# Kernel tuning notes

Measured on AMD Instinct MI355X. Metric: run time of the kernel, lower is better.

The kernel has to match this reference:

```python
import jax, jax.numpy as jnp
import numpy as np

EPS = 1e-06


def setup_inputs() -> dict:
    key = jax.random.key(0)
    k1, k2, k3 = jax.random.split(key, 3)
    N, L, H, D = 2, 2048, 8, 64
    return {
        "queries": jax.random.normal(k1, (N, L, H, D), dtype=jnp.float32),
        "keys": jax.random.normal(k2, (N, L, H, D), dtype=jnp.float32),
        "values": jax.random.normal(k3, (N, L, H, D), dtype=jnp.float32),
    }


def reference(queries, keys, values):
    # [N, L, H, D] -> [N, H, L, D]
    q = jnp.transpose(queries, (0, 2, 1, 3))
    k = jnp.transpose(keys, (0, 2, 1, 3))
    v = jnp.transpose(values, (0, 2, 1, 3))
    # kernel_method = sigmoid (applied to q and k only)
    q = jax.nn.sigmoid(q)
    k = jax.nn.sigmoid(k)
    L = q.shape[2]
    normal = (jnp.arange(L, dtype=q.dtype) + 1.0)[None, None, :]  # [1,1,L]

    sink_incoming = 1.0 / jnp.einsum('nhld,nhld->nhl', q + EPS, jnp.cumsum(k, axis=2) + EPS)
    source_outgoing = 1.0 / jnp.einsum('nhld,nhld->nhl', k + EPS, jnp.cumsum(q, axis=2) + EPS)
    sink_incoming = sink_incoming * normal
    source_outgoing = source_outgoing * normal

    conserved_sink = jnp.einsum(
        'nhld,nhld->nhl', q + EPS,
        jnp.cumsum(k * source_outgoing[..., None], axis=2) + EPS) / normal
    conserved_source = jnp.einsum(
        'nhld,nhld->nhl', k + EPS,
        jnp.cumsum(q * sink_incoming[..., None], axis=2) + EPS) / normal
    conserved_source = jnp.clip(conserved_source, -1.0, 1.0)

    sink_allocation = jax.nn.sigmoid(conserved_sink)
    conserved_source = jnp.exp(conserved_source)
    source_competition = conserved_source / jnp.cumsum(conserved_source, axis=-1) * normal

    # causal dot product: outer-product cumsum as in the original
    q_scaled = q * (sink_incoming / normal)[..., None]
    v_scaled = v * source_competition[..., None]
    kv = jnp.cumsum(jnp.einsum('nhld,nhlm->nhldm', k, v_scaled), axis=2)  # [N,H,L,D,M]
    qkv = jnp.einsum('nhld,nhldm->nhlm', q_scaled, kv)
    x = qkv * sink_allocation[..., None]
    # back to [N, L, H, M]
    return jnp.transpose(x, (0, 2, 1, 3))
```

## Files before the change

kernel.cpp:

```cpp
#include <hip/hip_runtime.h>
#include <math.h>

constexpr int Nn = 2, Hh = 8, Ll = 2048, Dd = 64;
constexpr int S  = Nn * Hh;
constexpr int C  = 64;
constexpr int NC = Ll / C;
constexpr int SC = S * NC;

constexpr int SB  = 72;
constexpr int SRP = 65;
constexpr int SS8 = 9;

#define EPSF 1e-6f
#define FLAG_MAGIC 0x5F3A9D21u

typedef __attribute__((ext_vector_type(8))) short short8;
typedef __attribute__((ext_vector_type(4))) float f32x4;
#define MFMA16(a, b, c) __builtin_amdgcn_mfma_f32_16x16x32_bf16(a, b, c, 0, 0, 0)

__device__ __forceinline__ float rcpf(float x) { return __builtin_amdgcn_rcpf(x); }
__device__ __forceinline__ float sigf(float x) { return rcpf(1.0f + __expf(-x)); }

__device__ __forceinline__ float waveRed(float v) {
#pragma unroll
    for (int off = 32; off > 0; off >>= 1) v += __shfl_xor(v, off, 64);
    return v;
}

__device__ __forceinline__ int gidx(int n, int l, int h, int d) {
    return ((n * Ll + l) * Hh + h) * Dd + d;
}

__device__ __forceinline__ float fc(const float4& v, int u) { return ((const float*)&v)[u]; }

__device__ __forceinline__ unsigned short f2bf(float x) {
    unsigned int u = __float_as_uint(x);
    unsigned int r = (u + 0x7fffu + ((u >> 16) & 1u)) >> 16;
    return (unsigned short)r;
}
__device__ __forceinline__ unsigned int pack2(float lo, float hi) {
    return (unsigned int)f2bf(lo) | ((unsigned int)f2bf(hi) << 16);
}
__device__ __forceinline__ float bf2f(unsigned short u) {
    return __uint_as_float(((unsigned int)u) << 16);
}
__device__ __forceinline__ float lo16(unsigned int x) { return __uint_as_float(x << 16); }
__device__ __forceinline__ float hi16(unsigned int x) { return __uint_as_float(x & 0xffff0000u); }
__device__ __forceinline__ void unpack8(const uint4& v, float* o) {
    o[0] = lo16(v.x); o[1] = hi16(v.x); o[2] = lo16(v.y); o[3] = hi16(v.y);
    o[4] = lo16(v.z); o[5] = hi16(v.z); o[6] = lo16(v.w); o[7] = hi16(v.w);
}

__device__ __forceinline__ void pubf(float* p, float v) {
    __hip_atomic_store((unsigned int*)p, __float_as_uint(v),
                       __ATOMIC_RELAXED, __HIP_MEMORY_SCOPE_AGENT);
}
__device__ __forceinline__ float rdf(const float* p) {
    return __uint_as_float(__hip_atomic_load((const unsigned int*)p,
                       __ATOMIC_RELAXED, __HIP_MEMORY_SCOPE_AGENT));
}
__device__ __forceinline__ void pubu(unsigned int* p, unsigned int v) {
    __hip_atomic_store(p, v, __ATOMIC_RELAXED, __HIP_MEMORY_SCOPE_AGENT);
}
__device__ __forceinline__ unsigned long long rd64(const void* p) {
    return __hip_atomic_load((const unsigned long long*)p,
                             __ATOMIC_RELAXED, __HIP_MEMORY_SCOPE_AGENT);
}
__device__ __forceinline__ void publish_flag(unsigned int* f, int t) {
    asm volatile("s_waitcnt vmcnt(0)" ::: "memory");
    __syncthreads();
    if (t == 0)
        __hip_atomic_store(f, FLAG_MAGIC, __ATOMIC_RELAXED, __HIP_MEMORY_SCOPE_AGENT);
}
__device__ __forceinline__ void wait_n(const unsigned int* f, int n, int t) {
    if (t < 64) {
        const bool need = (t < n);
        for (;;) {
            unsigned int v = need
                ? __hip_atomic_load(&f[t], __ATOMIC_RELAXED, __HIP_MEMORY_SCOPE_AGENT)
                : FLAG_MAGIC;
            if (__all(v == FLAG_MAGIC)) break;
            __builtin_amdgcn_s_sleep(8);
        }
    }
    __syncthreads();
}

__global__ __launch_bounds__(256, 2) void k_all(
        const float* __restrict__ Q, const float* __restrict__ K,
        const float* __restrict__ V,
        float* __restrict__ SK, float* __restrict__ SQ,
        float* __restrict__ SKso, float* __restrict__ SQsi,
        float* __restrict__ Tcs, float* __restrict__ KVT,
        unsigned short* __restrict__ KVpb, float* __restrict__ Out,
        unsigned int* __restrict__ f0, unsigned int* __restrict__ f1,
        unsigned int* __restrict__ f2, unsigned int* __restrict__ f3,
        unsigned int* __restrict__ f4) {
    __shared__ __align__(16) unsigned short sqB[C * SB];
    __shared__ __align__(16) unsigned short skB[C * SB];
    __shared__ __align__(16) unsigned short vsT[C * SB];
    __shared__ __align__(16) unsigned short stB[C * SB];
    __shared__ __align__(16) float Pun[4608];
    __shared__ float scrA[C * SS8], scrB[C * SS8];
    __shared__ float colK[C], colQ[C], pk[Dd], pq[Dd];
    __shared__ float lsi[C], lso[C], rw1[C], rw2[C], le[C], ecum[C], lsc[C], s2l[C];
    __shared__ float pcsv;

    const int b = blockIdx.x, s = b / NC, c = b % NC;
    const int n = s / Hh, h = s % Hh, t = threadIdx.x;
    const int w = t >> 6, lane = t & 63, mf = lane & 15, qq = lane >> 4;
    const int I0 = 16 * w;
    float* P = Pun;

    {
        int d0 = (4 * t) & 63, ig = t >> 4;
        float psk[4] = {0, 0, 0, 0}, psq[4] = {0, 0, 0, 0};
#pragma unroll
        for (int j = 0; j < 4; j++) {
            int i = ig + 16 * j;
            int id = gidx(n, c * C + i, h, d0);
            float4 q4 = *(const float4*)&Q[id];
            float4 k4 = *(const float4*)&K[id];
            float a0 = sigf(q4.x), a1 = sigf(q4.y), a2 = sigf(q4.z), a3 = sigf(q4.w);
            float b0 = sigf(k4.x), b1 = sigf(k4.y), b2 = sigf(k4.z), b3 = sigf(k4.w);
            *(uint2*)&sqB[i * SB + d0] = make_uint2(pack2(a0, a1), pack2(a2, a3));
            *(uint2*)&skB[i * SB + d0] = make_uint2(pack2(b0, b1), pack2(b2, b3));
            psq[0] += a0; psq[1] += a1; psq[2] += a2; psq[3] += a3;
            psk[0] += b0; psk[1] += b1; psk[2] += b2; psk[3] += b3;
        }
#pragma unroll
        for (int r = 0; r < 4; r++) {
            P[ig * 64 + d0 + r] = psk[r];
            P[1024 + ig * 64 + d0 + r] = psq[r];
        }
        int i0 = (t & 15) * 4, dt = (t >> 4) * 4;
        float4 vr[4];
#pragma unroll
        for (int r = 0; r < 4; r++)
            vr[r] = *(const float4*)&V[gidx(n, c * C + i0 + r, h, dt)];
#pragma unroll
        for (int u = 0; u < 4; u++)
            *(uint2*)&vsT[(dt + u) * SB + i0] = make_uint2(
                pack2(fc(vr[0], u), fc(vr[1], u)), pack2(fc(vr[2], u), fc(vr[3], u)));
    }
    __syncthreads();
    if (t < 64) {
        float v = 0.f;
#pragma unroll
        for (int g = 0; g < 16; g++) v += P[g * 64 + t];
        pubf(&SK[b * 64 + t], v);
    } else if (t < 128) {
        int d = t - 64; float v = 0.f;
#pragma unroll
        for (int g = 0; g < 16; g++) v += P[1024 + g * 64 + d];
        pubf(&SQ[b * 64 + d], v);
    }
    publish_flag(&f0[b], t);

    wait_n(&f0[s * NC], c, t);

    {
        int d = t & 63, g = t >> 6;
        float pa = 0.f, pb = 0.f;
#pragma unroll
        for (int u = 0; u < 8; u++) {
            int cp = g + 4 * u;
            float va = rdf(&SK[(s * NC + cp) * 64 + d]);
            float vb = rdf(&SQ[(s * NC + cp) * 64 + d]);
            pa += (cp < c) ? va : 0.f;
            pb += (cp < c) ? vb : 0.f;
        }
        P[2048 + g * 64 + d] = pa;
        P[2304 + g * 64 + d] = pb;
    }
#pragma unroll
    for (int j = 0; j < 2; j++) {
        int flat = 8 * t + 2048 * j, i = flat >> 6, d0 = flat & 63;
        uint4 xq = *(const uint4*)&sqB[i * SB + d0];
        uint4 xk = *(const uint4*)&skB[i * SB + d0];
        float qa[8], ka[8];
        unpack8(xq, qa); unpack8(xk, ka);
        float sq = 0.f, sk = 0.f;
#pragma unroll
        for (int u = 0; u < 8; u++) { sq += qa[u]; sk += ka[u]; }
        scrB[i * SS8 + (d0 >> 3)] = sq;
        scrA[i * SS8 + (d0 >> 3)] = sk;
    }
    __syncthreads();
    if (t < 64) {
        float v = 0.f;
#pragma unroll
        for (int u = 0; u < 8; u++) v += scrA[t * SS8 + u];
        colK[t] = v;
    } else if (t < 128) {
        int i = t - 64; float v = 0.f;
#pragma unroll
        for (int u = 0; u < 8; u++) v += scrB[i * SS8 + u];
        colQ[i] = v;
    } else if (t < 192) {
        int d = t - 128;
        pk[d] = P[2048 + d] + P[2112 + d] + P[2176 + d] + P[2240 + d];
    } else {
        int d = t - 192;
        pq[d] = P[2304 + d] + P[2368 + d] + P[2432 + d] + P[2496 + d];
    }
    __syncthreads();

    {
        f32x4 acc[4] = {{0,0,0,0},{0,0,0,0},{0,0,0,0},{0,0,0,0}};
#pragma unroll
        for (int kk = 0; kk < 64; kk += 32) {
            short8 a = *(const short8*)&sqB[(I0 + mf) * SB + kk + qq * 8];
#pragma unroll
            for (int J = 0; J < 4; J++) {
                short8 bb = *(const short8*)&skB[(16 * J + mf) * SB + kk + qq * 8];
                acc[J] = MFMA16(a, bb, acc[J]);
            }
        }
#pragma unroll
        for (int J = 0; J < 4; J++)
#pragma unroll
            for (int r = 0; r < 4; r++)
                P[(I0 + 4 * qq + r) * SRP + 16 * J + mf] = acc[J][r];
    }
    __syncthreads();

    {
        int i = t >> 2, g = t & 3, l = c * C + i;
        float r1 = 0.f, r2 = 0.f;
#pragma unroll
        for (int u = 0; u < 16; u++) {
            int jj = g + 4 * u;
            float t1 = P[i * SRP + jj] + EPSF * colK[jj];
            float t2 = P[jj * SRP + i] + EPSF * colQ[jj];
            bool ok = (jj <= i);
            r1 += ok ? t1 : 0.f;
            r2 += ok ? t2 : 0.f;
        }
        float b1 = 0.f, b2 = 0.f;
#pragma unroll
        for (int u = 0; u < 16; u++) {
            int d = g * 16 + u;
            b1 += (bf2f(sqB[i * SB + d]) + EPSF) * (pk[d] + EPSF);
            b2 += (bf2f(skB[i * SB + d]) + EPSF) * (pq[d] + EPSF);
        }
        r1 += __shfl_xor(r1, 1, 64); r1 += __shfl_xor(r1, 2, 64);
        r2 += __shfl_xor(r2, 1, 64); r2 += __shfl_xor(r2, 2, 64);
        b1 += __shfl_xor(b1, 1, 64); b1 += __shfl_xor(b1, 2, 64);
        b2 += __shfl_xor(b2, 1, 64); b2 += __shfl_xor(b2, 2, 64);
        if (g == 0) {
            float nf = (float)(l + 1);
            lsi[i] = nf * rcpf(b1 + r1);
            lso[i] = nf * rcpf(b2 + r2);
        }
    }
    __syncthreads();

    {
        int i = t >> 2, g = t & 3;
        float a1 = 0.f, a2 = 0.f;
#pragma unroll
        for (int u = 0; u < 16; u++) {
            int jj = g + 4 * u;
            float t1 = lso[jj] * (P[i * SRP + jj] + EPSF * colK[jj]);
            float t2 = lsi[jj] * (P[jj * SRP + i] + EPSF * colQ[jj]);
            bool ok = (jj <= i);
            a1 += ok ? t1 : 0.f;
            a2 += ok ? t2 : 0.f;
        }
        a1 += __shfl_xor(a1, 1, 64); a1 += __shfl_xor(a1, 2, 64);
        a2 += __shfl_xor(a2, 1, 64); a2 += __shfl_xor(a2, 2, 64);
        if (g == 0) { rw1[i] = a1; rw2[i] = a2; }
    }
    {
        int d = t >> 2, g = t & 3;
        float v1 = 0.f, v2 = 0.f;
#pragma unroll
        for (int u = 0; u < 16; u++) {
            int i = g * 16 + u;
            v1 += bf2f(skB[i * SB + d]) * lso[i];
            v2 += bf2f(sqB[i * SB + d]) * lsi[i];
        }
        v1 += __shfl_xor(v1, 1, 64); v1 += __shfl_xor(v1, 2, 64);
        v2 += __shfl_xor(v2, 1, 64); v2 += __shfl_xor(v2, 2, 64);
        if (g == 0) {
            pubf(&SKso[b * 64 + d], v1);
            pubf(&SQsi[b * 64 + d], v2);
        }
    }
    publish_flag(&f1[b], t);

    wait_n(&f1[s * NC], c, t);

    {
        int d = t & 63, g = t >> 6;
        float pa = 0.f, pb = 0.f;
#pragma unroll
        for (int u = 0; u < 8; u++) {
            int cp = g + 4 * u;
            float va = rdf(&SKso[(s * NC + cp) * 64 + d]);
            float vb = rdf(&SQsi[(s * NC + cp) * 64 + d]);
            pa += (cp < c) ? va : 0.f;
            pb += (cp < c) ? vb : 0.f;
        }
        scrA[g * 64 + d] = pa;
        scrA[256 + g * 64 + d] = pb;
    }
    __syncthreads();
    if (t < 64) pk[t] = scrA[t] + scrA[64 + t] + scrA[128 + t] + scrA[192 + t];
    else if (t < 128) {
        int d = t - 64;
        pq[d] = scrA[256 + d] + scrA[320 + d] + scrA[384 + d] + scrA[448 + d];
    }
    __syncthreads();
    {
        int i = t >> 2, g = t & 3, l = c * C + i;
        float b1 = 0.f, b2 = 0.f;
#pragma unroll
        for (int j = 0; j < 2; j++) {
            uint4 xq = *(const uint4*)&sqB[i * SB + g * 16 + 8 * j];
            uint4 xk = *(const uint4*)&skB[i * SB + g * 16 + 8 * j];
            float qa[8], ka[8];
            unpack8(xq, qa); unpack8(xk, ka);
            int d = g * 16 + 8 * j;
#pragma unroll
            for (int u = 0; u < 8; u++) {
                b1 += (qa[u] + EPSF) * (pk[d + u] + EPSF);
                b2 += (ka[u] + EPSF) * (pq[d + u] + EPSF);
            }
        }
        b1 += __shfl_xor(b1, 1, 64); b1 += __shfl_xor(b1, 2, 64);
        b2 += __shfl_xor(b2, 1, 64); b2 += __shfl_xor(b2, 2, 64);
        if (g == 0) {
            float nf = (float)(l + 1);
            float cs  = (b1 + rw1[i]) * rcpf(nf);
            float csr = (b2 + rw2[i]) * rcpf(nf);
            csr = fminf(fmaxf(csr, -1.f), 1.f);
            float e = __expf(csr);
            float sal = sigf(cs);
            s2l[i] = lsi[i] * rcpf(nf) * sal;
            le[i] = e;
        }
    }
    __syncthreads();
    if (t < 64) {
        float run = le[t];
#pragma unroll
        for (int off = 1; off < 64; off <<= 1) {
            float o = __shfl_up(run, off, 64);
            if (t >= off) run += o;
        }
        ecum[t] = run;
        if (t == 63) pubf(&Tcs[b], run);
    }
    publish_flag(&f2[b], t);

    wait_n(&f2[s * NC], c, t);

    if (t < 64) {
        float v = (t < c) ? rdf(&Tcs[s * NC + t]) : 0.f;
        v = waveRed(v);
        if (t == 0) pcsv = v;
    }
    __syncthreads();
    if (t < 64) {
        int l = c * C + t;
        lsc[t] = le[t] * rcpf(pcsv + ecum[t]) * (float)(l + 1);
    }
    __syncthreads();

    {
        int i = t >> 2, g = t & 3;
        unsigned int wds[8];
#pragma unroll
        for (int p = 0; p < 8; p++) {
            int j0 = g * 16 + 2 * p;
            float v0 = (j0     <= i) ? P[i * SRP + j0]     * lsc[j0]     : 0.f;
            float v1 = (j0 + 1 <= i) ? P[i * SRP + j0 + 1] * lsc[j0 + 1] : 0.f;
            wds[p] = pack2(v0, v1);
        }
        *(uint4*)&stB[i * SB + g * 16]     = make_uint4(wds[0], wds[1], wds[2], wds[3]);
        *(uint4*)&stB[i * SB + g * 16 + 8] = make_uint4(wds[4], wds[5], wds[6], wds[7]);
    }
    __syncthreads();

    unsigned short* skT = (unsigned short*)Pun;
    unsigned short* vsV = (unsigned short*)(Pun + 2304);
#pragma unroll
    for (int j = 0; j < 2; j++) {
        int flat = 8 * t + 2048 * j, dR = flat >> 6, i0 = flat & 63;
        uint4 vv = *(const uint4*)&vsT[dR * SB + i0];
        float x[8];
        unpack8(vv, x);
#pragma unroll
        for (int u = 0; u < 8; u++) x[u] *= lsc[i0 + u];
        uint4 o;
        o.x = pack2(x[0], x[1]); o.y = pack2(x[2], x[3]);
        o.z = pack2(x[4], x[5]); o.w = pack2(x[6], x[7]);
        *(uint4*)&vsV[dR * SB + i0] = o;
    }
    {
        int i0 = (t & 15) * 4, dt = (t >> 4) * 4;
        uint2 kr[4];
#pragma unroll
        for (int r = 0; r < 4; r++) kr[r] = *(const uint2*)&skB[(i0 + r) * SB + dt];
#pragma unroll
        for (int u = 0; u < 4; u++) {
            unsigned int e0 = (u < 2 ? kr[0].x : kr[0].y), e1 = (u < 2 ? kr[1].x : kr[1].y);
            unsigned int e2 = (u < 2 ? kr[2].x : kr[2].y), e3 = (u < 2 ? kr[3].x : kr[3].y);
            int sh = (u & 1) * 16;
            unsigned int lo = ((e0 >> sh) & 0xffffu) | (((e1 >> sh) & 0xffffu) << 16);
            unsigned int hi = ((e2 >> sh) & 0xffffu) | (((e3 >> sh) & 0xffffu) << 16);
            *(uint2*)&skT[(dt + u) * SB + i0] = make_uint2(lo, hi);
        }
    }
    __syncthreads();

    {
        f32x4 acc[4] = {{0,0,0,0},{0,0,0,0},{0,0,0,0},{0,0,0,0}};
#pragma unroll
        for (int kk = 0; kk < 64; kk += 32) {
            short8 a = *(const short8*)&vsV[(I0 + mf) * SB + kk + qq * 8];
#pragma unroll
            for (int J = 0; J < 4; J++) {
                short8 bb = *(const short8*)&skT[(16 * J + mf) * SB + kk + qq * 8];
                acc[J] = MFMA16(a, bb, acc[J]);
            }
        }
#pragma unroll
        for (int J = 0; J < 4; J++)
#pragma unroll
            for (int r = 0; r < 4; r++)
                pubf(&KVT[(size_t)b * 4096 + (I0 + 4 * qq + r) * 64 + 16 * J + mf],
                     acc[J][r]);
    }
    publish_flag(&f3[b], t);

    if (b < 128) {
        int sp = b >> 3, sub = b & 7;
        wait_n(&f3[sp * NC], NC, t);
        int e0 = sub * 512 + 2 * t;
        float2 x[NC];
#pragma unroll
        for (int cp = 0; cp < NC; cp++) {
            unsigned long long v = rd64(&KVT[(size_t)(sp * NC + cp) * 4096 + e0]);
            x[cp].x = __uint_as_float((unsigned int)v);
            x[cp].y = __uint_as_float((unsigned int)(v >> 32));
        }
        float r0 = 0.f, r1 = 0.f;
#pragma unroll
        for (int cp = 0; cp < NC; cp++) {
            pubu((unsigned int*)&KVpb[(size_t)(sp * NC + cp) * 4096 + e0], pack2(r0, r1));
            r0 += x[cp].x; r1 += x[cp].y;
        }
        publish_flag(&f4[b], t);
    }

    wait_n(&f4[8 * s], 8, t);
    unsigned long long kvp[4];
    size_t base = (size_t)b * 4096;
#pragma unroll
    for (int j = 0; j < 2; j++) {
        kvp[2 * j]     = rd64(&KVpb[base + 8 * t + 2048 * j]);
        kvp[2 * j + 1] = rd64(&KVpb[base + 8 * t + 2048 * j + 4]);
    }
#pragma unroll
    for (int j = 0; j < 2; j++) {
        int flat = 8 * t + 2048 * j, i = flat >> 6, d0 = flat & 63;
        *(uint2*)&skB[i * SB + d0] =
            make_uint2((unsigned int)kvp[2 * j], (unsigned int)(kvp[2 * j] >> 32));
        *(uint2*)&skB[i * SB + d0 + 4] =
            make_uint2((unsigned int)kvp[2 * j + 1], (unsigned int)(kvp[2 * j + 1] >> 32));
    }
    __syncthreads();

    {
        f32x4 acc[4] = {{0,0,0,0},{0,0,0,0},{0,0,0,0},{0,0,0,0}};
#pragma unroll
        for (int kk = 0; kk < 64; kk += 32) {
            short8 a1 = *(const short8*)&sqB[(I0 + mf) * SB + kk + qq * 8];
            short8 a2 = *(const short8*)&stB[(I0 + mf) * SB + kk + qq * 8];
#pragma unroll
            for (int J = 0; J < 4; J++) {
                short8 b1 = *(const short8*)&skB[(16 * J + mf) * SB + kk + qq * 8];
                acc[J] = MFMA16(a1, b1, acc[J]);
                short8 b2 = *(const short8*)&vsT[(16 * J + mf) * SB + kk + qq * 8];
                acc[J] = MFMA16(a2, b2, acc[J]);
            }
        }
#pragma unroll
        for (int J = 0; J < 4; J++)
#pragma unroll
            for (int r = 0; r < 4; r++) {
                int io = I0 + 4 * qq + r;
                Out[gidx(n, c * C + io, h, 16 * J + mf)] = acc[J][r] * s2l[io];
            }
    }
}

extern "C" void kernel_launch(void* const* d_in, const int* in_sizes, int n_in,
                              void* d_out, int out_size, void* d_ws, size_t ws_size,
                              hipStream_t stream) {
    const float* Q = (const float*)d_in[0];
    const float* K = (const float*)d_in[1];
    const float* V = (const float*)d_in[2];
    float* Out = (float*)d_out;

    float* ws   = (float*)d_ws;
    float* SK   = ws;
    float* SQ   = SK   + SC * 64;
    float* SKso = SQ   + SC * 64;
    float* SQsi = SKso + SC * 64;
    float* Tcs  = SQsi + SC * 64;
    float* KVT  = Tcs  + SC;
    unsigned short* KVpb = (unsigned short*)(KVT + (size_t)SC * 4096);
    unsigned int* f0 = (unsigned int*)(KVpb + (size_t)SC * 4096);
    unsigned int* f1 = f0 + SC;
    unsigned int* f2 = f1 + SC;
    unsigned int* f3 = f2 + SC;
    unsigned int* f4 = f3 + SC;

    k_all<<<SC, 256, 0, stream>>>(Q, K, V, SK, SQ, SKso, SQsi, Tcs, KVT, KVpb, Out,
                                  f0, f1, f2, f3, f4);
}
```

Before: 99.23 us.

## Replace two-stage KV prefix scan with direct per-block prefix summation

Previously 128 blocks read the per-chunk KV state matrices, computed an exclusive prefix across chunks into a bf16 buffer and signalled another flag that every block waited on. Now each block waits only for its own preceding chunks' flags and sums their fp32 KV matrices directly into shared memory, removing one global barrier stage and the intermediate buffer. The cost is redundant reads that grow with chunk index (up to 31 matrices for the last chunk), plain non-atomic loads of data published by other blocks, and a shorter spin-sleep interval.

```diff
diff --git a/kernel.cpp b/kernel.cpp
--- a/kernel.cpp
+++ b/kernel.cpp
@@ -58,13 +58,6 @@
 __device__ __forceinline__ float rdf(const float* p) {
     return __uint_as_float(__hip_atomic_load((const unsigned int*)p,
                        __ATOMIC_RELAXED, __HIP_MEMORY_SCOPE_AGENT));
-}
-__device__ __forceinline__ void pubu(unsigned int* p, unsigned int v) {
-    __hip_atomic_store(p, v, __ATOMIC_RELAXED, __HIP_MEMORY_SCOPE_AGENT);
-}
-__device__ __forceinline__ unsigned long long rd64(const void* p) {
-    return __hip_atomic_load((const unsigned long long*)p,
-                             __ATOMIC_RELAXED, __HIP_MEMORY_SCOPE_AGENT);
 }
 __device__ __forceinline__ void publish_flag(unsigned int* f, int t) {
     asm volatile("s_waitcnt vmcnt(0)" ::: "memory");
@@ -80,10 +73,11 @@
                 ? __hip_atomic_load(&f[t], __ATOMIC_RELAXED, __HIP_MEMORY_SCOPE_AGENT)
                 : FLAG_MAGIC;
             if (__all(v == FLAG_MAGIC)) break;
-            __builtin_amdgcn_s_sleep(8);
-        }
-    }
-    __syncthreads();
+            __builtin_amdgcn_s_sleep(1);
+        }
+    }
+    __syncthreads();
+    asm volatile("" ::: "memory");
 }
 
 __global__ __launch_bounds__(256, 2) void k_all(
@@ -92,10 +86,9 @@
         float* __restrict__ SK, float* __restrict__ SQ,
         float* __restrict__ SKso, float* __restrict__ SQsi,
         float* __restrict__ Tcs, float* __restrict__ KVT,
-        unsigned short* __restrict__ KVpb, float* __restrict__ Out,
+        float* __restrict__ Out,
         unsigned int* __restrict__ f0, unsigned int* __restrict__ f1,
-        unsigned int* __restrict__ f2, unsigned int* __restrict__ f3,
-        unsigned int* __restrict__ f4) {
+        unsigned int* __restrict__ f2, unsigned int* __restrict__ f3) {
     __shared__ __align__(16) unsigned short sqB[C * SB];
     __shared__ __align__(16) unsigned short skB[C * SB];
     __shared__ __align__(16) unsigned short vsT[C * SB];
@@ -436,41 +429,31 @@
     }
     publish_flag(&f3[b], t);
 
-    if (b < 128) {
-        int sp = b >> 3, sub = b & 7;
-        wait_n(&f3[sp * NC], NC, t);
-        int e0 = sub * 512 + 2 * t;
-        float2 x[NC];
-#pragma unroll
-        for (int cp = 0; cp < NC; cp++) {
-            unsigned long long v = rd64(&KVT[(size_t)(sp * NC + cp) * 4096 + e0]);
-            x[cp].x = __uint_as_float((unsigned int)v);
-            x[cp].y = __uint_as_float((unsigned int)(v >> 32));
-        }
-        float r0 = 0.f, r1 = 0.f;
-#pragma unroll
-        for (int cp = 0; cp < NC; cp++) {
-            pubu((unsigned int*)&KVpb[(size_t)(sp * NC + cp) * 4096 + e0], pack2(r0, r1));
-            r0 += x[cp].x; r1 += x[cp].y;
-        }
-        publish_flag(&f4[b], t);
-    }
-
-    wait_n(&f4[8 * s], 8, t);
-    unsigned long long kvp[4];
-    size_t base = (size_t)b * 4096;
-#pragma unroll
-    for (int j = 0; j < 2; j++) {
-        kvp[2 * j]     = rd64(&KVpb[base + 8 * t + 2048 * j]);
-        kvp[2 * j + 1] = rd64(&KVpb[base + 8 * t + 2048 * j + 4]);
-    }
-#pragma unroll
-    for (int j = 0; j < 2; j++) {
-        int flat = 8 * t + 2048 * j, i = flat >> 6, d0 = flat & 63;
-        *(uint2*)&skB[i * SB + d0] =
-            make_uint2((unsigned int)kvp[2 * j], (unsigned int)(kvp[2 * j] >> 32));
-        *(uint2*)&skB[i * SB + d0 + 4] =
-            make_uint2((unsigned int)kvp[2 * j + 1], (unsigned int)(kvp[2 * j + 1] >> 32));
+    wait_n(&f3[s * NC], c, t);
+    {
+        int m = t >> 2, dcol = (t & 3) * 16;
+        float racc[16];
+#pragma unroll
+        for (int u = 0; u < 16; u++) racc[u] = 0.f;
+        const float* Kb0 = &KVT[(size_t)(s * NC) * 4096 + m * 64 + dcol];
+        for (int cp = 0; cp < c; cp++) {
+            const float* Kp = Kb0 + (size_t)cp * 4096;
+            float4 x0 = *(const float4*)&Kp[0];
+            float4 x1 = *(const float4*)&Kp[4];
+            float4 x2 = *(const float4*)&Kp[8];
+            float4 x3 = *(const float4*)&Kp[12];
+            racc[0]  += x0.x; racc[1]  += x0.y; racc[2]  += x0.z; racc[3]  += x0.w;
+            racc[4]  += x1.x; racc[5]  += x1.y; racc[6]  += x1.z; racc[7]  += x1.w;
+            racc[8]  += x2.x; racc[9]  += x2.y; racc[10] += x2.z; racc[11] += x2.w;
+            racc[12] += x3.x; racc[13] += x3.y; racc[14] += x3.z; racc[15] += x3.w;
+        }
+        uint4 o0, o1;
+        o0.x = pack2(racc[0],  racc[1]);  o0.y = pack2(racc[2],  racc[3]);
+        o0.z = pack2(racc[4],  racc[5]);  o0.w = pack2(racc[6],  racc[7]);
+        o1.x = pack2(racc[8],  racc[9]);  o1.y = pack2(racc[10], racc[11]);
+        o1.z = pack2(racc[12], racc[13]); o1.w = pack2(racc[14], racc[15]);
+        *(uint4*)&skB[m * SB + dcol]     = o0;
+        *(uint4*)&skB[m * SB + dcol + 8] = o1;
     }
     __syncthreads();
 
@@ -513,13 +496,11 @@
     float* SQsi = SKso + SC * 64;
     float* Tcs  = SQsi + SC * 64;
     float* KVT  = Tcs  + SC;
-    unsigned short* KVpb = (unsigned short*)(KVT + (size_t)SC * 4096);
-    unsigned int* f0 = (unsigned int*)(KVpb + (size_t)SC * 4096);
+    unsigned int* f0 = (unsigned int*)(KVT + (size_t)SC * 4096);
     unsigned int* f1 = f0 + SC;
     unsigned int* f2 = f1 + SC;
     unsigned int* f3 = f2 + SC;
-    unsigned int* f4 = f3 + SC;
-
-    k_all<<<SC, 256, 0, stream>>>(Q, K, V, SK, SQ, SKso, SQsi, Tcs, KVT, KVpb, Out,
-                                  f0, f1, f2, f3, f4);
-}
+
+    k_all<<<SC, 256, 0, stream>>>(Q, K, V, SK, SQ, SKso, SQsi, Tcs, KVT, Out,
+                                  f0, f1, f2, f3);
+}
```

New measurement: 106.8 us. +7.6%, slower.

## Pack chunk exp-sum into 64-bit flag, reuse P values in registers, localize prefix-scan blocks

Applied to the files above, without the earlier changes.

The per-chunk exp cumulative total is now stored together with the ready flag in one 64-bit atomic. This removes the separate Tcs store, the vmcnt wait and the extra barrier before the flag is published, and lets waiters read the value straight from the flag. P row and column values are kept in registers so the second masked reduction does not reload them from shared memory. The KV prefix-scan work moves from blocks 0-127 to the blocks with c<8 inside each sequence, so the scanning blocks belong to the same head as their consumers, which may change scheduling locality. Risks include the ordering of the combined 64-bit flag and extra register pressure.

```diff
diff --git a/kernel.cpp b/kernel.cpp
--- a/kernel.cpp
+++ b/kernel.cpp
@@ -84,6 +84,7 @@
         }
     }
     __syncthreads();
+    asm volatile("" ::: "memory");
 }
 
 __global__ __launch_bounds__(256, 2) void k_all(
@@ -91,10 +92,10 @@
         const float* __restrict__ V,
         float* __restrict__ SK, float* __restrict__ SQ,
         float* __restrict__ SKso, float* __restrict__ SQsi,
-        float* __restrict__ Tcs, float* __restrict__ KVT,
-        unsigned short* __restrict__ KVpb, float* __restrict__ Out,
+        float* __restrict__ KVT, unsigned short* __restrict__ KVpb,
+        float* __restrict__ Out,
         unsigned int* __restrict__ f0, unsigned int* __restrict__ f1,
-        unsigned int* __restrict__ f2, unsigned int* __restrict__ f3,
+        unsigned long long* __restrict__ f2, unsigned int* __restrict__ f3,
         unsigned int* __restrict__ f4) {
     __shared__ __align__(16) unsigned short sqB[C * SB];
     __shared__ __align__(16) unsigned short skB[C * SB];
@@ -227,15 +228,16 @@
 
     {
         int i = t >> 2, g = t & 3, l = c * C + i;
+        float prow[16], pcol[16];
         float r1 = 0.f, r2 = 0.f;
 #pragma unroll
         for (int u = 0; u < 16; u++) {
             int jj = g + 4 * u;
-            float t1 = P[i * SRP + jj] + EPSF * colK[jj];
-            float t2 = P[jj * SRP + i] + EPSF * colQ[jj];
+            prow[u] = P[i * SRP + jj] + EPSF * colK[jj];
+            pcol[u] = P[jj * SRP + i] + EPSF * colQ[jj];
             bool ok = (jj <= i);
-            r1 += ok ? t1 : 0.f;
-            r2 += ok ? t2 : 0.f;
+            r1 += ok ? prow[u] : 0.f;
+            r2 += ok ? pcol[u] : 0.f;
         }
         float b1 = 0.f, b2 = 0.f;
 #pragma unroll
@@ -253,17 +255,14 @@
             lsi[i] = nf * rcpf(b1 + r1);
             lso[i] = nf * rcpf(b2 + r2);
         }
-    }
-    __syncthreads();
-
-    {
-        int i = t >> 2, g = t & 3;
+        __syncthreads();
+
         float a1 = 0.f, a2 = 0.f;
 #pragma unroll
         for (int u = 0; u < 16; u++) {
             int jj = g + 4 * u;
-            float t1 = lso[jj] * (P[i * SRP + jj] + EPSF * colK[jj]);
-            float t2 = lsi[jj] * (P[jj * SRP + i] + EPSF * colQ[jj]);
+            float t1 = lso[jj] * prow[u];
+            float t2 = lsi[jj] * pcol[u];
             bool ok = (jj <= i);
             a1 += ok ? t1 : 0.f;
             a2 += ok ? t2 : 0.f;
@@ -351,18 +350,32 @@
             if (t >= off) run += o;
         }
         ecum[t] = run;
-        if (t == 63) pubf(&Tcs[b], run);
-    }
-    publish_flag(&f2[b], t);
-
-    wait_n(&f2[s * NC], c, t);
+    }
+    __syncthreads();
+    if (t == 0) {
+        unsigned long long pv = ((unsigned long long)FLAG_MAGIC << 32)
+                              | (unsigned long long)__float_as_uint(ecum[63]);
+        __hip_atomic_store(&f2[b], pv, __ATOMIC_RELAXED, __HIP_MEMORY_SCOPE_AGENT);
+    }
 
     if (t < 64) {
-        float v = (t < c) ? rdf(&Tcs[s * NC + t]) : 0.f;
-        v = waveRed(v);
+        bool need = (t < c);
+        float tv = 0.f;
+        for (;;) {
+            unsigned long long x = need
+                ? __hip_atomic_load(&f2[s * NC + t], __ATOMIC_RELAXED, __HIP_MEMORY_SCOPE_AGENT)
+                : ((unsigned long long)FLAG_MAGIC << 32);
+            if (__all((unsigned int)(x >> 32) == FLAG_MAGIC)) {
+                tv = need ? __uint_as_float((unsigned int)x) : 0.f;
+                break;
+            }
+            __builtin_amdgcn_s_sleep(8);
+        }
+        float v = waveRed(tv);
         if (t == 0) pcsv = v;
     }
     __syncthreads();
+
     if (t < 64) {
         int l = c * C + t;
         lsc[t] = le[t] * rcpf(pcsv + ecum[t]) * (float)(l + 1);
@@ -436,24 +449,23 @@
     }
     publish_flag(&f3[b], t);
 
-    if (b < 128) {
-        int sp = b >> 3, sub = b & 7;
-        wait_n(&f3[sp * NC], NC, t);
-        int e0 = sub * 512 + 2 * t;
+    if (c < 8) {
+        wait_n(&f3[s * NC], NC, t);
+        int e0 = c * 512 + 2 * t;
         float2 x[NC];
 #pragma unroll
         for (int cp = 0; cp < NC; cp++) {
-            unsigned long long v = rd64(&KVT[(size_t)(sp * NC + cp) * 4096 + e0]);
+            unsigned long long v = rd64(&KVT[(size_t)(s * NC + cp) * 4096 + e0]);
             x[cp].x = __uint_as_float((unsigned int)v);
             x[cp].y = __uint_as_float((unsigned int)(v >> 32));
         }
         float r0 = 0.f, r1 = 0.f;
 #pragma unroll
         for (int cp = 0; cp < NC; cp++) {
-            pubu((unsigned int*)&KVpb[(size_t)(sp * NC + cp) * 4096 + e0], pack2(r0, r1));
+            pubu((unsigned int*)&KVpb[(size_t)(s * NC + cp) * 4096 + e0], pack2(r0, r1));
             r0 += x[cp].x; r1 += x[cp].y;
         }
-        publish_flag(&f4[b], t);
+        publish_flag(&f4[s * 8 + c], t);
     }
 
     wait_n(&f4[8 * s], 8, t);
@@ -511,15 +523,14 @@
     float* SQ   = SK   + SC * 64;
     float* SKso = SQ   + SC * 64;
     float* SQsi = SKso + SC * 64;
-    float* Tcs  = SQsi + SC * 64;
-    float* KVT  = Tcs  + SC;
+    float* KVT  = SQsi + SC * 64;
     unsigned short* KVpb = (unsigned short*)(KVT + (size_t)SC * 4096);
-    unsigned int* f0 = (unsigned int*)(KVpb + (size_t)SC * 4096);
+    unsigned long long* f2 = (unsigned long long*)(KVpb + (size_t)SC * 4096);
+    unsigned int* f0 = (unsigned int*)(f2 + SC);
     unsigned int* f1 = f0 + SC;
-    unsigned int* f2 = f1 + SC;
-    unsigned int* f3 = f2 + SC;
+    unsigned int* f3 = f1 + SC;
     unsigned int* f4 = f3 + SC;
 
-    k_all<<<SC, 256, 0, stream>>>(Q, K, V, SK, SQ, SKso, SQsi, Tcs, KVT, KVpb, Out,
+    k_all<<<SC, 256, 0, stream>>>(Q, K, V, SK, SQ, SKso, SQsi, KVT, KVpb, Out,
                                   f0, f1, f2, f3, f4);
 }
```

After: 99.54 us. Within noise of the previous version (+0.3%).
